# Optimization experiments

Measured on AMD Instinct MI355X. Metric: run time of the kernel, lower is better.

The kernel has to match this reference:

```python
import jax, jax.numpy as jnp
import numpy as np

B, S, D, H = 2, 2048, 1024, 16
DK = D // H


def setup_inputs() -> dict:
    key = jax.random.key(0)
    ks = jax.random.split(key, 11)
    s = 1.0 / np.sqrt(D)
    inp = {
        "q": jax.random.normal(ks[0], (B, S, D), jnp.float32),
        "k": jax.random.normal(ks[1], (B, S, D), jnp.float32),
        "v": jax.random.normal(ks[2], (B, S, D), jnp.float32),
        "mask": jnp.tril(jnp.ones((S, S), jnp.int32))[None, None],  # [1,1,S,S] causal
        "wq": jax.random.normal(ks[3], (D, D), jnp.float32) * s,
        "bq": jax.random.normal(ks[4], (D,), jnp.float32) * s,
        "wk": jax.random.normal(ks[5], (D, D), jnp.float32) * s,
        "bk": jax.random.normal(ks[6], (D,), jnp.float32) * s,
        "wv": jax.random.normal(ks[7], (D, D), jnp.float32) * s,
        "bv": jax.random.normal(ks[8], (D,), jnp.float32) * s,
        "wo": jax.random.normal(ks[9], (D, D), jnp.float32) * s,
        "bo": jax.random.normal(ks[10], (D,), jnp.float32) * s,
    }
    return inp


def reference(q, k, v, mask, wq, bq, wk, bk, wv, bv, wo, bo):
    # Linear projections (torch Linear: x @ W.T + b)
    def split_heads(x):  # [B,S,D] -> [B,H,S,DK]
        return x.reshape(B, S, H, DK).transpose(0, 2, 1, 3)

    query = split_heads(q @ wq.T + bq)
    key_ = split_heads(k @ wk.T + bk)
    value = split_heads(v @ wv.T + bv)

    scale = 1.0 / jnp.sqrt(jnp.asarray(DK, q.dtype))
    scores = jnp.einsum("bhqd,bhkd->bhqk", query, key_) * scale
    scores = jnp.where(mask == 0, jnp.asarray(-1e9, scores.dtype), scores)
    attn = jax.nn.softmax(scores, axis=-1)  # dropout=0.0 -> identity
    x = jnp.einsum("bhqk,bhkd->bhqd", attn, value)
    x = x.transpose(0, 2, 1, 3).reshape(B, S, D)
    return x @ wo.T + bo
```

## Files before the change

### kernel.cpp

```cpp
#include <hip/hip_runtime.h>

typedef unsigned short u16;
typedef __bf16 bf16x8 __attribute__((ext_vector_type(8)));
typedef u16 u16x8 __attribute__((ext_vector_type(8)));
typedef float f32x4 __attribute__((ext_vector_type(4)));

constexpr size_t WQo = 12582912;
constexpr size_t WOo = 15728640;
constexpr size_t QPo = 16777216;
constexpr size_t KPo = 20971520;
constexpr size_t VTo = 25165824;
constexpr size_t OOo = 29360128;

#define GLD(g, l) __builtin_amdgcn_global_load_lds( \
    (const __attribute__((address_space(1))) void*)(g), \
    (__attribute__((address_space(3))) void*)(l), 16, 0, 0)

__device__ __forceinline__ u16 f2bf(float f) {
  unsigned u = __builtin_bit_cast(unsigned, f);
  u += 0x7fffu + ((u >> 16) & 1u);
  return (u16)(u >> 16);
}

__device__ __forceinline__ f32x4 zero4() {
  f32x4 z = {0.f, 0.f, 0.f, 0.f};
  return z;
}

__device__ __forceinline__ f32x4 mfma16(u16x8 a, u16x8 b, f32x4 c) {
  return __builtin_amdgcn_mfma_f32_16x16x32_bf16(
      __builtin_bit_cast(bf16x8, a), __builtin_bit_cast(bf16x8, b), c, 0, 0, 0);
}

__global__ __launch_bounds__(256) void cast_all(
    const float4* __restrict__ q, const float4* __restrict__ k, const float4* __restrict__ v,
    const float4* __restrict__ wq, const float4* __restrict__ wk,
    const float4* __restrict__ wv, const float4* __restrict__ wo,
    ushort4* __restrict__ dst)
{
  int i = blockIdx.x * 256 + threadIdx.x;
  constexpr int QN = 1048576;
  constexpr int WN = 262144;
  float4 val;
  if (i < QN)            val = q[i];
  else if (i < 2 * QN)   val = k[i - QN];
  else if (i < 3 * QN)   val = v[i - 2 * QN];
  else {
    int j = i - 3 * QN;
    if (j < WN)          val = wq[j];
    else if (j < 2 * WN) val = wk[j - WN];
    else if (j < 3 * WN) val = wv[j - 2 * WN];
    else                 val = wo[j - 3 * WN];
  }
  ushort4 o;
  o.x = f2bf(val.x); o.y = f2bf(val.y); o.z = f2bf(val.z); o.w = f2bf(val.w);
  dst[i] = o;
}

template <int TM>
__device__ __forceinline__ void gemm_core(
    const u16* __restrict__ A, const u16* __restrict__ W,
    const float* __restrict__ bias, void* __restrict__ outp, int mode)
{
  constexpr int Kd = 1024;
  constexpr int BM = TM * 32;
  constexpr int ACALLS = BM * 8 / 256;
  __shared__ u16 As[BM * 64];
  __shared__ u16 Bs[128 * 64];
  const int tid = threadIdx.x;
  const int wave = tid >> 6, lane = tid & 63;
  const int q4 = lane >> 4, l15 = lane & 15;
  const int m0 = blockIdx.y * BM, n0 = blockIdx.x * 128;
  const int wm = (wave >> 1) * (TM * 16), wn = (wave & 1) * 64;

  f32x4 acc[TM][4];
#pragma unroll
  for (int i = 0; i < TM; ++i)
#pragma unroll
    for (int j = 0; j < 4; ++j) acc[i][j] = zero4();

  for (int kt = 0; kt < Kd; kt += 64) {
#pragma unroll
    for (int t = 0; t < ACALLS; ++t) {
      const int pos = t * 256 + wave * 64 + lane;
      const int row = pos >> 3, c = (pos & 7) ^ (row & 7);
      GLD(A + (size_t)(m0 + row) * Kd + kt + c * 8, As + t * 2048 + wave * 512);
    }
#pragma unroll
    for (int t = 0; t < 4; ++t) {
      const int pos = t * 256 + wave * 64 + lane;
      const int row = pos >> 3, c = (pos & 7) ^ (row & 7);
      GLD(W + (size_t)(n0 + row) * Kd + kt + c * 8, Bs + t * 2048 + wave * 512);
    }
    __syncthreads();
#pragma unroll
    for (int h = 0; h < 2; ++h) {
      u16x8 af[TM], bfv[4];
#pragma unroll
      for (int i = 0; i < TM; ++i) {
        const int row = wm + i * 16 + l15;
        const int p = (h * 4 + q4) ^ (row & 7);
        af[i] = *(const u16x8*)&As[row * 64 + p * 8];
      }
#pragma unroll
      for (int j = 0; j < 4; ++j) {
        const int row = wn + j * 16 + l15;
        const int p = (h * 4 + q4) ^ (row & 7);
        bfv[j] = *(const u16x8*)&Bs[row * 64 + p * 8];
      }
#pragma unroll
      for (int i = 0; i < TM; ++i)
#pragma unroll
        for (int j = 0; j < 4; ++j)
          acc[i][j] = mfma16(af[i], bfv[j], acc[i][j]);
    }
    __syncthreads();
  }

#pragma unroll
  for (int i = 0; i < TM; ++i) {
    const int mb = m0 + wm + i * 16 + q4 * 4;
#pragma unroll
    for (int j = 0; j < 4; ++j) {
      const int col = n0 + wn + j * 16 + l15;
      const float bsv = bias[col];
      if (mode == 1) {
        const int bb = mb >> 11, s = mb & 2047, hh = col >> 6, dk = col & 63;
        ushort4 pk;
        pk.x = f2bf(acc[i][j][0] + bsv);
        pk.y = f2bf(acc[i][j][1] + bsv);
        pk.z = f2bf(acc[i][j][2] + bsv);
        pk.w = f2bf(acc[i][j][3] + bsv);
        *(ushort4*)&((u16*)outp)[((size_t)(bb * 16 + hh) * 64 + dk) * 2048 + s] = pk;
      } else {
#pragma unroll
        for (int r = 0; r < 4; ++r) {
          const float val = acc[i][j][r] + bsv;
          const int m = mb + r;
          if (mode == 0) {
            const int bb = m >> 11, s = m & 2047, hh = col >> 6, dk = col & 63;
            ((u16*)outp)[((size_t)(bb * 16 + hh) * 2048 + s) * 64 + dk] = f2bf(val);
          } else {
            ((float*)outp)[(size_t)m * 1024 + col] = val;
          }
        }
      }
    }
  }
}

__global__ __launch_bounds__(256) void proj_gemm(
    u16* __restrict__ ws, const float* __restrict__ bq,
    const float* __restrict__ bk, const float* __restrict__ bv)
{
  const int z = blockIdx.z;
  const u16* A = ws + (size_t)z * 4194304;
  const u16* W = ws + WQo + (size_t)z * 1048576;
  const float* bias = (z == 0) ? bq : ((z == 1) ? bk : bv);
  u16* outp = ws + QPo + (size_t)z * 4194304;
  gemm_core<4>(A, W, bias, outp, (z == 2) ? 1 : 0);
}

__global__ __launch_bounds__(256) void out_gemm(
    const u16* __restrict__ ws, const float* __restrict__ bo, float* __restrict__ out)
{
  gemm_core<2>(ws + OOo, ws + WOo, bo, out, 3);
}

__global__ __launch_bounds__(256) void flash_attn(u16* __restrict__ ws)
{
  constexpr int S = 2048;
  const int a = blockIdx.x;
  const int b = 31 - blockIdx.x;
  const int bh = blockIdx.y;
  const int bb = bh >> 4, h = bh & 15;
  const int tid = threadIdx.x;
  const int wave = tid >> 6, lane = tid & 63;
  const int q4 = lane >> 4, l15 = lane & 15;

  __shared__ u16 QsA[64 * 64];
  __shared__ u16 QsB[64 * 64];
  __shared__ u16 Ks[2][64 * 64];
  __shared__ u16 Vs[2][64 * 64];

  const u16* Qg = ws + QPo + (size_t)bh * S * 64;
  const u16* Kg = ws + KPo + (size_t)bh * S * 64;
  const u16* Vg = ws + VTo + (size_t)bh * 64 * S;
  u16* Og = ws + OOo;

  const int ch0 = wave * 128 + lane;
  const int ch1 = ch0 + 64;
  const int r0 = ch0 >> 3, c0 = (ch0 & 7) ^ (r0 & 7);
  const int r1 = ch1 >> 3, c1 = (ch1 & 7) ^ (r1 & 7);

  GLD(Qg + (size_t)(a * 64 + r0) * 64 + c0 * 8, QsA + wave * 1024);
  GLD(Qg + (size_t)(a * 64 + r1) * 64 + c1 * 8, QsA + wave * 1024 + 512);
  GLD(Qg + (size_t)(b * 64 + r0) * 64 + c0 * 8, QsB + wave * 1024);
  GLD(Qg + (size_t)(b * 64 + r1) * 64 + c1 * 8, QsB + wave * 1024 + 512);
  GLD(Kg + (size_t)r0 * 64 + c0 * 8, Ks[0] + wave * 1024);
  GLD(Kg + (size_t)r1 * 64 + c1 * 8, Ks[0] + wave * 1024 + 512);
  GLD(Vg + (size_t)r0 * S + c0 * 8, Vs[0] + wave * 1024);
  GLD(Vg + (size_t)r1 * S + c1 * 8, Vs[0] + wave * 1024 + 512);
  __syncthreads();

  u16x8 qfA[2], qfB[2];
  {
    const int row = wave * 16 + l15;
#pragma unroll
    for (int kk = 0; kk < 2; ++kk) {
      const int c = (kk * 4 + q4) ^ (row & 7);
      qfA[kk] = *(const u16x8*)&QsA[row * 64 + c * 8];
      qfB[kk] = *(const u16x8*)&QsB[row * 64 + c * 8];
    }
  }
  u16* Ps = QsA + wave * 1024;

  f32x4 oA[4], oB[4];
  float lA[4], lB[4];
#pragma unroll
  for (int j = 0; j < 4; ++j) { oA[j] = zero4(); oB[j] = zero4(); }
#pragma unroll
  for (int r = 0; r < 4; ++r) { lA[r] = 0.f; lB[r] = 0.f; }

  for (int kt = 0; kt <= b; ++kt) {
    const u16* Ksb = Ks[kt & 1];
    const u16* Vsb = Vs[kt & 1];
    if (kt < b) {
      const u16* Kt = Kg + (size_t)(kt + 1) * 64 * 64;
      u16* Kd = Ks[(kt + 1) & 1];
      u16* Vd = Vs[(kt + 1) & 1];
      GLD(Kt + (size_t)r0 * 64 + c0 * 8, Kd + wave * 1024);
      GLD(Kt + (size_t)r1 * 64 + c1 * 8, Kd + wave * 1024 + 512);
      GLD(Vg + (size_t)r0 * S + (kt + 1) * 64 + c0 * 8, Vd + wave * 1024);
      GLD(Vg + (size_t)r1 * S + (kt + 1) * 64 + c1 * 8, Vd + wave * 1024 + 512);
    }

    auto process = [&](const u16x8* qf, f32x4* o_acc, float* l_p, int qt, bool diag) {
      f32x4 sf[4];
#pragma unroll
      for (int j = 0; j < 4; ++j) {
        f32x4 z = zero4();
        const int row = j * 16 + l15;
#pragma unroll
        for (int kk = 0; kk < 2; ++kk) {
          const int c = (kk * 4 + q4) ^ (row & 7);
          z = mfma16(qf[kk], *(const u16x8*)&Ksb[row * 64 + c * 8], z);
        }
        sf[j] = z;
      }
      if (diag) {
        const int rowg0 = qt * 64 + wave * 16 + q4 * 4;
#pragma unroll
        for (int j = 0; j < 4; ++j) {
          const int colg = kt * 64 + j * 16 + l15;
#pragma unroll
          for (int r = 0; r < 4; ++r) {
            float val = sf[j][r] * 0.125f;
            if (colg > rowg0 + r) val = -__builtin_inff();
            sf[j][r] = __expf(val);
          }
        }
      } else {
#pragma unroll
        for (int j = 0; j < 4; ++j)
#pragma unroll
          for (int r = 0; r < 4; ++r)
            sf[j][r] = __expf(sf[j][r] * 0.125f);
      }
#pragma unroll
      for (int j = 0; j < 4; ++j)
#pragma unroll
        for (int r = 0; r < 4; ++r) l_p[r] += sf[j][r];

#pragma unroll
      for (int j = 0; j < 4; ++j)
#pragma unroll
        for (int r = 0; r < 4; ++r) {
          const int m = q4 * 4 + r;
          const int srow = j * 16 + l15;
          const int pos = m * 64 + (((srow >> 3) ^ (m & 7)) << 3) + (srow & 7);
          Ps[pos] = f2bf(sf[j][r]);
        }
      u16x8 pf[2];
#pragma unroll
      for (int kk = 0; kk < 2; ++kk) {
        const int c = (kk * 4 + q4) ^ (l15 & 7);
        pf[kk] = *(const u16x8*)&Ps[l15 * 64 + c * 8];
      }
#pragma unroll
      for (int j = 0; j < 4; ++j) {
        const int row = j * 16 + l15;
#pragma unroll
        for (int kk = 0; kk < 2; ++kk) {
          const int c = (kk * 4 + q4) ^ (row & 7);
          o_acc[j] = mfma16(pf[kk], *(const u16x8*)&Vsb[row * 64 + c * 8], o_acc[j]);
        }
      }
    };

    process(qfB, oB, lB, b, kt == b);
    if (kt <= a) process(qfA, oA, lA, a, kt == a);
    __syncthreads();
  }

#pragma unroll
  for (int off = 1; off < 16; off <<= 1)
#pragma unroll
    for (int r = 0; r < 4; ++r) {
      lA[r] += __shfl_xor(lA[r], off, 64);
      lB[r] += __shfl_xor(lB[r], off, 64);
    }

#pragma unroll
  for (int r = 0; r < 4; ++r) {
    const float invA = 1.f / lA[r];
    const float invB = 1.f / lB[r];
    const int sA = a * 64 + wave * 16 + q4 * 4 + r;
    const int sB = b * 64 + wave * 16 + q4 * 4 + r;
    const size_t baseA = ((size_t)(bb * 2048 + sA)) * 1024 + h * 64;
    const size_t baseB = ((size_t)(bb * 2048 + sB)) * 1024 + h * 64;
#pragma unroll
    for (int j = 0; j < 4; ++j) {
      Og[baseA + j * 16 + l15] = f2bf(oA[j][r] * invA);
      Og[baseB + j * 16 + l15] = f2bf(oB[j][r] * invB);
    }
  }
}

extern "C" void kernel_launch(void* const* d_in, const int* in_sizes, int n_in,
                              void* d_out, int out_size, void* d_ws, size_t ws_size,
                              hipStream_t stream)
{
  const float* q  = (const float*)d_in[0];
  const float* k  = (const float*)d_in[1];
  const float* v  = (const float*)d_in[2];
  const float* wq = (const float*)d_in[4];
  const float* bq = (const float*)d_in[5];
  const float* wk = (const float*)d_in[6];
  const float* bk = (const float*)d_in[7];
  const float* wv = (const float*)d_in[8];
  const float* bv = (const float*)d_in[9];
  const float* wo = (const float*)d_in[10];
  const float* bo = (const float*)d_in[11];
  u16* ws = (u16*)d_ws;
  float* out = (float*)d_out;

  cast_all<<<16384, 256, 0, stream>>>(
      (const float4*)q, (const float4*)k, (const float4*)v,
      (const float4*)wq, (const float4*)wk, (const float4*)wv, (const float4*)wo,
      (ushort4*)ws);
  proj_gemm<<<dim3(8, 32, 3), 256, 0, stream>>>(ws, bq, bk, bv);
  flash_attn<<<dim3(16, 32), 256, 0, stream>>>(ws);
  out_gemm<<<dim3(8, 64), 256, 0, stream>>>(ws, bo, out);
}
```

Baseline: 236.6 us.

## Halve GEMM K-tile to 32 with packed swizzled LDS and linearized block order

The projection and output GEMMs now step through K in tiles of 32 instead of 64. Two rows are packed into each 64-element LDS line with an XOR swizzle, which halves shared memory per block and should allow more resident blocks per CU. Both grids are flattened to 1D with the M index varying fastest, so neighbouring blocks share the same weight tile and get better L2 reuse. The trade-off is twice as many K iterations and barriers, with less MFMA work between each pair of syncs.

Result: no change. 237.8 us (+0.5%).

```diff
diff --git a/kernel.cpp b/kernel.cpp
--- a/kernel.cpp
+++ b/kernel.cpp
@@ -60,17 +60,17 @@
 template <int TM>
 __device__ __forceinline__ void gemm_core(
     const u16* __restrict__ A, const u16* __restrict__ W,
-    const float* __restrict__ bias, void* __restrict__ outp, int mode)
+    const float* __restrict__ bias, void* __restrict__ outp,
+    int m0, int n0, int mode)
 {
   constexpr int Kd = 1024;
   constexpr int BM = TM * 32;
-  constexpr int ACALLS = BM * 8 / 256;
-  __shared__ u16 As[BM * 64];
-  __shared__ u16 Bs[128 * 64];
+  constexpr int ACALLS = BM / 64;
+  __shared__ u16 As[BM * 32];
+  __shared__ u16 Bs[128 * 32];
   const int tid = threadIdx.x;
   const int wave = tid >> 6, lane = tid & 63;
   const int q4 = lane >> 4, l15 = lane & 15;
-  const int m0 = blockIdx.y * BM, n0 = blockIdx.x * 128;
   const int wm = (wave >> 1) * (TM * 16), wn = (wave & 1) * 64;
 
   f32x4 acc[TM][4];
@@ -79,41 +79,44 @@
 #pragma unroll
     for (int j = 0; j < 4; ++j) acc[i][j] = zero4();
 
-  for (int kt = 0; kt < Kd; kt += 64) {
+  for (int kt = 0; kt < Kd; kt += 32) {
 #pragma unroll
     for (int t = 0; t < ACALLS; ++t) {
       const int pos = t * 256 + wave * 64 + lane;
-      const int row = pos >> 3, c = (pos & 7) ^ (row & 7);
-      GLD(A + (size_t)(m0 + row) * Kd + kt + c * 8, As + t * 2048 + wave * 512);
-    }
-#pragma unroll
-    for (int t = 0; t < 4; ++t) {
+      const int lr = pos >> 3, p = pos & 7;
+      const int c = p ^ (lr & 7);
+      const int m = lr * 2 + (c >> 2), k4 = c & 3;
+      GLD(A + (size_t)(m0 + m) * Kd + kt + k4 * 8, As + t * 2048 + wave * 512);
+    }
+#pragma unroll
+    for (int t = 0; t < 2; ++t) {
       const int pos = t * 256 + wave * 64 + lane;
-      const int row = pos >> 3, c = (pos & 7) ^ (row & 7);
-      GLD(W + (size_t)(n0 + row) * Kd + kt + c * 8, Bs + t * 2048 + wave * 512);
+      const int lr = pos >> 3, p = pos & 7;
+      const int c = p ^ (lr & 7);
+      const int m = lr * 2 + (c >> 2), k4 = c & 3;
+      GLD(W + (size_t)(n0 + m) * Kd + kt + k4 * 8, Bs + t * 2048 + wave * 512);
     }
     __syncthreads();
-#pragma unroll
-    for (int h = 0; h < 2; ++h) {
-      u16x8 af[TM], bfv[4];
-#pragma unroll
-      for (int i = 0; i < TM; ++i) {
-        const int row = wm + i * 16 + l15;
-        const int p = (h * 4 + q4) ^ (row & 7);
-        af[i] = *(const u16x8*)&As[row * 64 + p * 8];
-      }
-#pragma unroll
-      for (int j = 0; j < 4; ++j) {
-        const int row = wn + j * 16 + l15;
-        const int p = (h * 4 + q4) ^ (row & 7);
-        bfv[j] = *(const u16x8*)&Bs[row * 64 + p * 8];
-      }
-#pragma unroll
-      for (int i = 0; i < TM; ++i)
-#pragma unroll
-        for (int j = 0; j < 4; ++j)
-          acc[i][j] = mfma16(af[i], bfv[j], acc[i][j]);
-    }
+    u16x8 af[TM], bfv[4];
+#pragma unroll
+    for (int i = 0; i < TM; ++i) {
+      const int m = wm + i * 16 + l15;
+      const int lr = m >> 1;
+      const int p = ((m & 1) * 4 + q4) ^ (lr & 7);
+      af[i] = *(const u16x8*)&As[lr * 64 + p * 8];
+    }
+#pragma unroll
+    for (int j = 0; j < 4; ++j) {
+      const int m = wn + j * 16 + l15;
+      const int lr = m >> 1;
+      const int p = ((m & 1) * 4 + q4) ^ (lr & 7);
+      bfv[j] = *(const u16x8*)&Bs[lr * 64 + p * 8];
+    }
+#pragma unroll
+    for (int i = 0; i < TM; ++i)
+#pragma unroll
+      for (int j = 0; j < 4; ++j)
+        acc[i][j] = mfma16(af[i], bfv[j], acc[i][j]);
     __syncthreads();
   }
 
@@ -153,18 +156,22 @@
     u16* __restrict__ ws, const float* __restrict__ bq,
     const float* __restrict__ bk, const float* __restrict__ bv)
 {
-  const int z = blockIdx.z;
+  const int id = blockIdx.x;
+  const int z = id >> 8, rem = id & 255;
+  const int bx = rem >> 5, by = rem & 31;
   const u16* A = ws + (size_t)z * 4194304;
   const u16* W = ws + WQo + (size_t)z * 1048576;
   const float* bias = (z == 0) ? bq : ((z == 1) ? bk : bv);
   u16* outp = ws + QPo + (size_t)z * 4194304;
-  gemm_core<4>(A, W, bias, outp, (z == 2) ? 1 : 0);
+  gemm_core<4>(A, W, bias, outp, by * 128, bx * 128, (z == 2) ? 1 : 0);
 }
 
 __global__ __launch_bounds__(256) void out_gemm(
     const u16* __restrict__ ws, const float* __restrict__ bo, float* __restrict__ out)
 {
-  gemm_core<2>(ws + OOo, ws + WOo, bo, out, 3);
+  const int id = blockIdx.x;
+  const int bx = id >> 6, by = id & 63;
+  gemm_core<2>(ws + OOo, ws + WOo, bo, out, by * 64, bx * 128, 3);
 }
 
 __global__ __launch_bounds__(256) void flash_attn(u16* __restrict__ ws)
@@ -349,7 +356,7 @@
       (const float4*)q, (const float4*)k, (const float4*)v,
       (const float4*)wq, (const float4*)wk, (const float4*)wv, (const float4*)wo,
       (ushort4*)ws);
-  proj_gemm<<<dim3(8, 32, 3), 256, 0, stream>>>(ws, bq, bk, bv);
+  proj_gemm<<<768, 256, 0, stream>>>(ws, bq, bk, bv);
   flash_attn<<<dim3(16, 32), 256, 0, stream>>>(ws);
-  out_gemm<<<dim3(8, 64), 256, 0, stream>>>(ws, bo, out);
-}
+  out_gemm<<<512, 256, 0, stream>>>(ws, bo, out);
+}
```
